# Optimization experiments

Hardware: AMD Instinct MI355X
Metric: run time of the kernel (lower is better)

## Reference

```python
import jax, jax.numpy as jnp
import numpy as np

SEG_LENS = [2048, 8192]
DIL_RATES = [1, 2]


def _dilated_attention(q, k, v, is_causal):
    # q,k,v: [b, n, h, d]
    b, n, h, d = q.shape
    ng = len(SEG_LENS)
    g = h // ng  # heads per group (even split)
    scale = 1.0 / np.sqrt(d).astype(np.float32)
    out = jnp.zeros_like(q)
    for i, (s, r) in enumerate(zip(SEG_LENS, DIL_RATES)):
        hs = i * g
        offset = i % r  # offset_idx % dilation_rate, as in _create_dilation_pattern
        idx = np.arange(offset, s, r)  # dilated positions within a segment, length m
        m = idx.shape[0]
        ns = n // s  # number of segments
        # reshape to segments then gather dilated positions: [b, ns, m, g, d]
        qg = q[:, :, hs:hs + g, :].reshape(b, ns, s, g, d)[:, :, idx]
        kg = k[:, :, hs:hs + g, :].reshape(b, ns, s, g, d)[:, :, idx]
        vg = v[:, :, hs:hs + g, :].reshape(b, ns, s, g, d)[:, :, idx]
        # segment-local attention over dilated tokens only (structured sparsity)
        scores = jnp.einsum('bsqhd,bskhd->bshqk', qg, kg) * scale
        if is_causal:
            cm = np.tril(np.ones((m, m), dtype=bool))  # idx is sorted -> causal in dilated order
            scores = jnp.where(cm, scores, -jnp.inf)
        attn = jax.nn.softmax(scores, axis=-1)
        og = jnp.einsum('bshqk,bskhd->bsqhd', attn, vg)  # [b, ns, m, g, d]
        # scatter back to full segment positions; non-dilated positions stay zero
        full = jnp.zeros((b, ns, s, g, d), q.dtype).at[:, :, idx].set(og)
        out = out.at[:, :, hs:hs + g, :].set(full.reshape(b, n, g, d))
    return out


def setup_inputs() -> dict:
    key = jax.random.key(0)
    k1, k2, k3 = jax.random.split(key, 3)
    shape = (1, 8192, 8, 64)
    q = jax.random.normal(k1, shape, dtype=jnp.float32)
    k = jax.random.normal(k2, shape, dtype=jnp.float32)
    v = jax.random.normal(k3, shape, dtype=jnp.float32)
    return {"q": q, "k": k, "v": v, "is_causal": 1}


def reference(q, k, v, is_causal):
    return _dilated_attention(q, k, v, bool(is_causal))
```

## Files before the change

### kernel.cpp

```cpp
#include <hip/hip_runtime.h>


#define LP 72

typedef __attribute__((ext_vector_type(8))) short bf16x8;
typedef __attribute__((ext_vector_type(4))) float f32x4;
typedef __attribute__((ext_vector_type(4))) unsigned u32x4;
typedef const unsigned int __attribute__((address_space(1)))* gp1;
typedef unsigned int __attribute__((address_space(3)))* lp3;

__device__ __forceinline__ unsigned short f2bf(float f) {
  unsigned u = __builtin_bit_cast(unsigned, f);
  u += 0x7fff + ((u >> 16) & 1);
  return (unsigned short)(u >> 16);
}

__device__ __forceinline__ int region_base(int head) {
  return (head < 4) ? head * 524288 : 2097152 + (head - 4) * 262144;
}

__device__ __forceinline__ void gl_lds16(const unsigned short* g, unsigned short* l) {
  __builtin_amdgcn_global_load_lds((gp1)g, (lp3)l, 16, 0, 0);
}

__global__ __launch_bounds__(256, 4)
void prep_kernel(const float* __restrict__ K, const float* __restrict__ V,
                 unsigned short* __restrict__ Kb, unsigned short* __restrict__ Vt) {
  __shared__ unsigned short sT[64][LP];
  const int bid = blockIdx.x;
  int head, pos0, rate, off;
  if (bid < 512) { head = bid >> 7; pos0 = (bid & 127) * 64; rate = 1; off = 0; }
  else { int b = bid - 512; head = 4 + (b >> 6); pos0 = (b & 63) * 64; rate = 2; off = 1; }
  const int rb = region_base(head);
  const int tid = threadIdx.x;
  const int row = tid >> 2, dg = tid & 3;
  const long tok = (long)(pos0 + row) * rate + off;

  {
    const float* kp = K + tok * 512 + head * 64 + dg * 16;
    unsigned short tmp[16];
    #pragma unroll
    for (int i = 0; i < 4; ++i) {
      float4 f = ((const float4*)kp)[i];
      tmp[i * 4 + 0] = f2bf(f.x); tmp[i * 4 + 1] = f2bf(f.y);
      tmp[i * 4 + 2] = f2bf(f.z); tmp[i * 4 + 3] = f2bf(f.w);
    }
    const int s = row & 7;
    unsigned short* dstrow = Kb + rb + (long)(pos0 + row) * 64;
    *(int4*)(dstrow + (((2 * dg)     ^ s) * 8)) = ((int4*)tmp)[0];
    *(int4*)(dstrow + (((2 * dg + 1) ^ s) * 8)) = ((int4*)tmp)[1];
  }

  {
    const float* vp = V + tok * 512 + head * 64 + dg * 16;
    #pragma unroll
    for (int i = 0; i < 4; ++i) {
      float4 f = ((const float4*)vp)[i];
      unsigned* p = (unsigned*)&sT[row][dg * 16 + i * 4];
      p[0] = (unsigned)f2bf(f.x) | ((unsigned)f2bf(f.y) << 16);
      p[1] = (unsigned)f2bf(f.z) | ((unsigned)f2bf(f.w) << 16);
    }
  }
  __syncthreads();

  {
    const int wv = tid >> 6, lane = tid & 63;
    unsigned pk[8];
    #pragma unroll
    for (int j = 0; j < 8; ++j) {
      unsigned lo = sT[wv * 16 + 2 * j][lane];
      unsigned hi = sT[wv * 16 + 2 * j + 1][lane];
      pk[j] = lo | (hi << 16);
    }
    const int s = lane & 7;
    unsigned short* dstrow = Vt + rb + (long)pos0 * 64 + lane * 64;
    int4 a = {(int)pk[0], (int)pk[1], (int)pk[2], (int)pk[3]};
    int4 b = {(int)pk[4], (int)pk[5], (int)pk[6], (int)pk[7]};
    *(int4*)(dstrow + (((2 * wv)     ^ s) * 8)) = a;
    *(int4*)(dstrow + (((2 * wv + 1) ^ s) * 8)) = b;
  }
}

__global__ __launch_bounds__(256, 2)
void attn_kernel(const float* __restrict__ Q, const unsigned short* __restrict__ Kb,
                 const unsigned short* __restrict__ Vt, const int* __restrict__ IC,
                 float* __restrict__ O, float* __restrict__ Slots) {
  __shared__ __attribute__((aligned(16))) unsigned short sK[2][4096];
  __shared__ __attribute__((aligned(16))) unsigned short sV[2][4096];

  const int bid = blockIdx.x;
  int head, q0, seg0, mseg, rate, off, grp, chunk, slot;
  if (bid < 512) {
    int h4 = bid & 3;
    int u = bid >> 2;
    chunk = u >> 6;
    int t = 63 - (u & 63);
    head = 4 + h4; seg0 = 0; mseg = 4096;
    rate = 2; off = 1; grp = 1;
    q0 = t * 64;
    slot = (h4 * 64 + t) * 2 + chunk;
  } else {
    int cc = bid - 512;
    int job = (cc & 7) | ((cc >> 8) << 3);
    int tloc = (cc & 255) >> 3;
    head = job & 3;
    seg0 = (job >> 2) * 2048;
    q0 = seg0 + tloc * 64; mseg = 2048;
    rate = 1; off = 0; grp = 0; chunk = 0; slot = 0;
  }
  const int rb = region_base(head);
  const bool causal = (*IC) != 0;
  const int tid = threadIdx.x, wave = tid >> 6, lane = tid & 63;
  const int l16 = lane & 15, quad = lane >> 4;
  const int ch0 = ((quad ^ (l16 & 7)) * 8);
  const int ch1 = ch0 ^ 32;

  const int qloc = q0 - seg0;
  const int diagkb = qloc >> 6;
  const int nkb = causal ? diagkb + 1 : (mseg >> 6);
  const int klo = grp ? chunk * 32 : 0;
  const int khi = grp ? min(nkb, klo + 32) : nkb;
  if (klo >= khi) return;

  const float QSCALE = 0.18033688011112042f;
  bf16x8 aQ[2];
  {
    long tok = (long)(q0 + wave * 16 + l16) * rate + off;
    const float* qp = Q + tok * 512 + head * 64 + quad * 8;
    #pragma unroll
    for (int kc = 0; kc < 2; ++kc) {
      float4 f0 = ((const float4*)(qp + kc * 32))[0];
      float4 f1 = ((const float4*)(qp + kc * 32))[1];
      bf16x8 a;
      a[0] = (short)f2bf(f0.x * QSCALE); a[1] = (short)f2bf(f0.y * QSCALE);
      a[2] = (short)f2bf(f0.z * QSCALE); a[3] = (short)f2bf(f0.w * QSCALE);
      a[4] = (short)f2bf(f1.x * QSCALE); a[5] = (short)f2bf(f1.y * QSCALE);
      a[6] = (short)f2bf(f1.z * QSCALE); a[7] = (short)f2bf(f1.w * QSCALE);
      aQ[kc] = a;
    }
  }

  f32x4 oacc[4];
  float lsum = 0.f;
  #pragma unroll
  for (int dt = 0; dt < 4; ++dt) oacc[dt] = (f32x4){0.f, 0.f, 0.f, 0.f};

  const unsigned short* Ksrc = Kb + rb + (long)seg0 * 64;
  const unsigned short* Vsrc = Vt + rb + (long)seg0 * 64;

  const int o0 = wave * 1024;
  const int lo = lane * 8;
  {
    const unsigned short* kt = Ksrc + (long)klo * 4096;
    const unsigned short* vt = Vsrc + (long)klo * 4096;
    gl_lds16(kt + o0 + lo,       &sK[0][o0]);
    gl_lds16(kt + o0 + 512 + lo, &sK[0][o0 + 512]);
    gl_lds16(vt + o0 + lo,       &sV[0][o0]);
    gl_lds16(vt + o0 + 512 + lo, &sV[0][o0 + 512]);
  }

  const int qv = qloc + wave * 16 + l16;

  for (int kb = klo; kb < khi; ++kb) {
    const int cur = (kb - klo) & 1;
    __syncthreads();
    if (kb + 1 < khi) {
      const unsigned short* kt = Ksrc + (long)(kb + 1) * 4096;
      const unsigned short* vt = Vsrc + (long)(kb + 1) * 4096;
      gl_lds16(kt + o0 + lo,       &sK[cur ^ 1][o0]);
      gl_lds16(kt + o0 + 512 + lo, &sK[cur ^ 1][o0 + 512]);
      gl_lds16(vt + o0 + lo,       &sV[cur ^ 1][o0]);
      gl_lds16(vt + o0 + 512 + lo, &sV[cur ^ 1][o0 + 512]);
    }
    const unsigned short* kbuf = &sK[cur][0];
    const unsigned short* vbuf = &sV[cur][0];

    f32x4 sc[4];
    #pragma unroll
    for (int c = 0; c < 4; ++c) {
      const unsigned short* krow = &kbuf[(c * 16 + l16) * 64];
      bf16x8 b0 = *(const bf16x8*)(krow + ch0);
      bf16x8 b1 = *(const bf16x8*)(krow + ch1);
      f32x4 z = (f32x4){0.f, 0.f, 0.f, 0.f};
      z = __builtin_amdgcn_mfma_f32_16x16x32_bf16(b0, aQ[0], z, 0, 0, 0);
      z = __builtin_amdgcn_mfma_f32_16x16x32_bf16(b1, aQ[1], z, 0, 0, 0);
      sc[c] = z;
    }

    float p[4][4];
    if (causal && (kb == diagkb)) {
      #pragma unroll
      for (int c = 0; c < 4; ++c)
        #pragma unroll
        for (int r = 0; r < 4; ++r) {
          float e = __builtin_amdgcn_exp2f(sc[c][r]);
          if (kb * 64 + c * 16 + quad * 4 + r > qv) e = 0.f;
          p[c][r] = e;
        }
    } else {
      #pragma unroll
      for (int c = 0; c < 4; ++c)
        #pragma unroll
        for (int r = 0; r < 4; ++r)
          p[c][r] = __builtin_amdgcn_exp2f(sc[c][r]);
    }

    lsum += (((p[0][0] + p[0][1]) + (p[0][2] + p[0][3])) +
             ((p[1][0] + p[1][1]) + (p[1][2] + p[1][3]))) +
            (((p[2][0] + p[2][1]) + (p[2][2] + p[2][3])) +
             ((p[3][0] + p[3][1]) + (p[3][2] + p[3][3])));

    unsigned W00, W01, W10, W11, W20, W21, W30, W31;
    asm("v_cvt_pk_bf16_f32 %0, %1, %2" : "=v"(W00) : "v"(p[0][0]), "v"(p[0][1]));
    asm("v_cvt_pk_bf16_f32 %0, %1, %2" : "=v"(W01) : "v"(p[0][2]), "v"(p[0][3]));
    asm("v_cvt_pk_bf16_f32 %0, %1, %2" : "=v"(W10) : "v"(p[1][0]), "v"(p[1][1]));
    asm("v_cvt_pk_bf16_f32 %0, %1, %2" : "=v"(W11) : "v"(p[1][2]), "v"(p[1][3]));
    asm("v_cvt_pk_bf16_f32 %0, %1, %2" : "=v"(W20) : "v"(p[2][0]), "v"(p[2][1]));
    asm("v_cvt_pk_bf16_f32 %0, %1, %2" : "=v"(W21) : "v"(p[2][2]), "v"(p[2][3]));
    asm("v_cvt_pk_bf16_f32 %0, %1, %2" : "=v"(W30) : "v"(p[3][0]), "v"(p[3][1]));
    asm("v_cvt_pk_bf16_f32 %0, %1, %2" : "=v"(W31) : "v"(p[3][2]), "v"(p[3][3]));

    unsigned R0 = W00, R2 = W10;
    asm("v_permlane32_swap_b32 %0, %1" : "+v"(R0), "+v"(R2));
    asm("v_permlane16_swap_b32 %0, %1" : "+v"(R0), "+v"(R2));
    unsigned R1 = W01, R3 = W11;
    asm("v_permlane32_swap_b32 %0, %1" : "+v"(R1), "+v"(R3));
    asm("v_permlane16_swap_b32 %0, %1" : "+v"(R1), "+v"(R3));
    unsigned R4 = W20, R6 = W30;
    asm("v_permlane32_swap_b32 %0, %1" : "+v"(R4), "+v"(R6));
    asm("v_permlane16_swap_b32 %0, %1" : "+v"(R4), "+v"(R6));
    unsigned R5 = W21, R7 = W31;
    asm("v_permlane32_swap_b32 %0, %1" : "+v"(R5), "+v"(R7));
    asm("v_permlane16_swap_b32 %0, %1" : "+v"(R5), "+v"(R7));
    u32x4 t0 = {R0, R1, R2, R3};
    u32x4 t1 = {R4, R5, R6, R7};
    bf16x8 pB0 = __builtin_bit_cast(bf16x8, t0);
    bf16x8 pB1 = __builtin_bit_cast(bf16x8, t1);

    #pragma unroll
    for (int dt = 0; dt < 4; ++dt) {
      const unsigned short* vrow = &vbuf[(dt * 16 + l16) * 64];
      bf16x8 v0 = *(const bf16x8*)(vrow + ch0);
      bf16x8 v1 = *(const bf16x8*)(vrow + ch1);
      oacc[dt] = __builtin_amdgcn_mfma_f32_16x16x32_bf16(v0, pB0, oacc[dt], 0, 0, 0);
      oacc[dt] = __builtin_amdgcn_mfma_f32_16x16x32_bf16(v1, pB1, oacc[dt], 0, 0, 0);
    }
  }

  float ltot = lsum;
  ltot += __shfl_xor(ltot, 16);
  ltot += __shfl_xor(ltot, 32);

  if (grp == 1) {
    float* S = Slots + (long)slot * 4160;
    const int qrow = wave * 16 + l16;
    #pragma unroll
    for (int dt = 0; dt < 4; ++dt)
      #pragma unroll
      for (int r = 0; r < 4; ++r)
        S[qrow * 64 + dt * 16 + quad * 4 + r] = oacc[dt][r];
    if (quad == 0) S[4096 + qrow] = ltot;
  } else {
    const int tq = q0 + wave * 16 + l16;
    const float inv = 1.0f / ltot;
    float* dst = O + (long)tq * 512 + head * 64 + quad * 4;
    #pragma unroll
    for (int dt = 0; dt < 4; ++dt)
      #pragma unroll
      for (int r = 0; r < 4; ++r)
        dst[dt * 16 + r] = oacc[dt][r] * inv;
  }
}

__global__ __launch_bounds__(256, 4)
void combine_kernel(const float* __restrict__ Slots, const int* __restrict__ IC,
                    float* __restrict__ O) {
  const int b = blockIdx.x;
  const int h4 = b >> 6, t = b & 63;
  const bool causal = (*IC) != 0;
  const int nkb = causal ? t + 1 : 64;
  const int nc = (nkb > 32) ? 2 : 1;
  const float* s0 = Slots + (long)((h4 * 64 + t) * 2) * 4160;
  const int tid = threadIdx.x;
  const int row = tid >> 2, dq = (tid & 3) * 16;

  float4 acc[4];
  const float4* p0 = (const float4*)(s0 + row * 64 + dq);
  #pragma unroll
  for (int i = 0; i < 4; ++i) acc[i] = p0[i];
  float l = s0[4096 + row];
  if (nc == 2) {
    const float* s1 = s0 + 4160;
    const float4* p1 = (const float4*)(s1 + row * 64 + dq);
    #pragma unroll
    for (int i = 0; i < 4; ++i) {
      float4 v = p1[i];
      acc[i].x += v.x; acc[i].y += v.y; acc[i].z += v.z; acc[i].w += v.w;
    }
    l += s1[4096 + row];
  }
  const float inv = 1.0f / l;
  const long tok = (long)(t * 64 + row) * 2 + 1;
  float* dst = O + tok * 512 + (4 + h4) * 64 + dq;
  #pragma unroll
  for (int i = 0; i < 4; ++i) {
    float4 o = {acc[i].x * inv, acc[i].y * inv, acc[i].z * inv, acc[i].w * inv};
    ((float4*)dst)[i] = o;
  }
  float* dste = O + (tok - 1) * 512 + (4 + h4) * 64 + dq;
  const float4 z = {0.f, 0.f, 0.f, 0.f};
  #pragma unroll
  for (int i = 0; i < 4; ++i) ((float4*)dste)[i] = z;
}

extern "C" void kernel_launch(void* const* d_in, const int* in_sizes, int n_in,
                              void* d_out, int out_size, void* d_ws, size_t ws_size,
                              hipStream_t stream) {
  const float* q = (const float*)d_in[0];
  const float* k = (const float*)d_in[1];
  const float* v = (const float*)d_in[2];
  const int* ic = (const int*)d_in[3];
  unsigned short* Kb = (unsigned short*)d_ws;
  unsigned short* Vt = Kb + 3145728;
  float* Slots = (float*)((char*)d_ws + 12582912);
  prep_kernel<<<dim3(768), dim3(256), 0, stream>>>(k, v, Kb, Vt);
  attn_kernel<<<dim3(1024), dim3(256), 0, stream>>>(q, Kb, Vt, ic, (float*)d_out, Slots);
  combine_kernel<<<dim3(256), dim3(256), 0, stream>>>(Slots, ic, (float*)d_out);
}
```

Measured before the change: 128.9 us.

## Triple-buffer K and split K/V waits to deepen load pipeline

Restructures the attention main loop into a software pipeline where K tiles are triple-buffered and prefetched two blocks ahead, while V is double-buffered and prefetched one ahead. Each iteration now has two barriers with explicit vmcnt waits, one before QK and one before PV, so the V load overlaps the QK/softmax phase instead of both landing before the block starts. This adds LDS usage (an extra 8KB K buffer) and a second barrier per iteration, which could affect occupancy or add sync cost.

```diff
diff --git a/kernel.cpp b/kernel.cpp
--- a/kernel.cpp
+++ b/kernel.cpp
@@ -81,11 +81,15 @@
   }
 }
 
+#define WAITV(n) asm volatile("s_waitcnt vmcnt(" #n ")" ::: "memory")
+#define BARRIER() do { __builtin_amdgcn_s_barrier(); \
+                       __builtin_amdgcn_sched_barrier(0); } while (0)
+
 __global__ __launch_bounds__(256, 2)
 void attn_kernel(const float* __restrict__ Q, const unsigned short* __restrict__ Kb,
                  const unsigned short* __restrict__ Vt, const int* __restrict__ IC,
                  float* __restrict__ O, float* __restrict__ Slots) {
-  __shared__ __attribute__((aligned(16))) unsigned short sK[2][4096];
+  __shared__ __attribute__((aligned(16))) unsigned short sK[3][4096];
   __shared__ __attribute__((aligned(16))) unsigned short sV[2][4096];
 
   const int bid = blockIdx.x;
@@ -150,31 +154,21 @@
 
   const int o0 = wave * 1024;
   const int lo = lane * 8;
-  {
-    const unsigned short* kt = Ksrc + (long)klo * 4096;
-    const unsigned short* vt = Vsrc + (long)klo * 4096;
-    gl_lds16(kt + o0 + lo,       &sK[0][o0]);
-    gl_lds16(kt + o0 + 512 + lo, &sK[0][o0 + 512]);
-    gl_lds16(vt + o0 + lo,       &sV[0][o0]);
-    gl_lds16(vt + o0 + 512 + lo, &sV[0][o0 + 512]);
-  }
-
   const int qv = qloc + wave * 16 + l16;
 
-  for (int kb = klo; kb < khi; ++kb) {
-    const int cur = (kb - klo) & 1;
-    __syncthreads();
-    if (kb + 1 < khi) {
-      const unsigned short* kt = Ksrc + (long)(kb + 1) * 4096;
-      const unsigned short* vt = Vsrc + (long)(kb + 1) * 4096;
-      gl_lds16(kt + o0 + lo,       &sK[cur ^ 1][o0]);
-      gl_lds16(kt + o0 + 512 + lo, &sK[cur ^ 1][o0 + 512]);
-      gl_lds16(vt + o0 + lo,       &sV[cur ^ 1][o0]);
-      gl_lds16(vt + o0 + 512 + lo, &sV[cur ^ 1][o0 + 512]);
-    }
-    const unsigned short* kbuf = &sK[cur][0];
-    const unsigned short* vbuf = &sV[cur][0];
-
+  auto stage_k = [&](int x, int sl) {
+    const unsigned short* kt = Ksrc + (long)x * 4096;
+    gl_lds16(kt + o0 + lo,       &sK[sl][o0]);
+    gl_lds16(kt + o0 + 512 + lo, &sK[sl][o0 + 512]);
+  };
+  auto stage_v = [&](int x) {
+    const unsigned short* vt = Vsrc + (long)x * 4096;
+    gl_lds16(vt + o0 + lo,       &sV[x & 1][o0]);
+    gl_lds16(vt + o0 + 512 + lo, &sV[x & 1][o0 + 512]);
+  };
+
+  struct PB { bf16x8 b0, b1; };
+  auto qk_phase = [&](int kb, const unsigned short* kbuf) -> PB {
     f32x4 sc[4];
     #pragma unroll
     for (int c = 0; c < 4; ++c) {
@@ -234,17 +228,61 @@
     asm("v_permlane16_swap_b32 %0, %1" : "+v"(R5), "+v"(R7));
     u32x4 t0 = {R0, R1, R2, R3};
     u32x4 t1 = {R4, R5, R6, R7};
-    bf16x8 pB0 = __builtin_bit_cast(bf16x8, t0);
-    bf16x8 pB1 = __builtin_bit_cast(bf16x8, t1);
-
+    PB pb;
+    pb.b0 = __builtin_bit_cast(bf16x8, t0);
+    pb.b1 = __builtin_bit_cast(bf16x8, t1);
+    return pb;
+  };
+
+  auto pv_phase = [&](const unsigned short* vbuf, PB pb) {
     #pragma unroll
     for (int dt = 0; dt < 4; ++dt) {
       const unsigned short* vrow = &vbuf[(dt * 16 + l16) * 64];
       bf16x8 v0 = *(const bf16x8*)(vrow + ch0);
       bf16x8 v1 = *(const bf16x8*)(vrow + ch1);
-      oacc[dt] = __builtin_amdgcn_mfma_f32_16x16x32_bf16(v0, pB0, oacc[dt], 0, 0, 0);
-      oacc[dt] = __builtin_amdgcn_mfma_f32_16x16x32_bf16(v1, pB1, oacc[dt], 0, 0, 0);
-    }
+      oacc[dt] = __builtin_amdgcn_mfma_f32_16x16x32_bf16(v0, pb.b0, oacc[dt], 0, 0, 0);
+      oacc[dt] = __builtin_amdgcn_mfma_f32_16x16x32_bf16(v1, pb.b1, oacc[dt], 0, 0, 0);
+    }
+  };
+
+  int kb = klo;
+  int kcur = klo % 3;
+  int ks2 = (klo + 2) % 3;
+  stage_k(klo, kcur);
+  stage_v(klo);
+  if (klo + 1 < khi) stage_k(klo + 1, kcur == 2 ? 0 : kcur + 1);
+
+  while (kb + 2 < khi) {
+    WAITV(4);
+    BARRIER();
+    stage_v(kb + 1);
+    stage_k(kb + 2, ks2);
+    PB pb = qk_phase(kb, &sK[kcur][0]);
+    WAITV(6);
+    BARRIER();
+    pv_phase(&sV[kb & 1][0], pb);
+    ++kb;
+    kcur = kcur == 2 ? 0 : kcur + 1;
+    ks2  = ks2  == 2 ? 0 : ks2  + 1;
+  }
+  if (kb + 1 < khi) {
+    WAITV(4);
+    BARRIER();
+    stage_v(kb + 1);
+    PB pb = qk_phase(kb, &sK[kcur][0]);
+    WAITV(4);
+    BARRIER();
+    pv_phase(&sV[kb & 1][0], pb);
+    ++kb;
+    kcur = kcur == 2 ? 0 : kcur + 1;
+  }
+  {
+    WAITV(2);
+    BARRIER();
+    PB pb = qk_phase(kb, &sK[kcur][0]);
+    WAITV(0);
+    BARRIER();
+    pv_phase(&sV[kb & 1][0], pb);
   }
 
   float ltot = lsum;
```

Result: no change. 130.9 us (+1.5%).

## Load V fragments directly from global into registers, drop V LDS staging

Applied to the files above, without the earlier changes.

The V-transpose kernel now writes V in a fragment-ordered layout that matches the MFMA operand order. The attention loop then reads each lane's eight 16-byte V fragments straight from global memory into registers instead of staging V through double-buffered LDS. This halves LDS use and removes the V LDS reads, which may allow higher occupancy. In exchange, every wave issues redundant global loads of the same V tile each iteration, and those loads sit in the critical path with no prefetch ahead of the QK phase.

```diff
diff --git a/kernel.cpp b/kernel.cpp
--- a/kernel.cpp
+++ b/kernel.cpp
@@ -72,12 +72,13 @@
       unsigned hi = sT[wv * 16 + 2 * j + 1][lane];
       pk[j] = lo | (hi << 16);
     }
-    const int s = lane & 7;
-    unsigned short* dstrow = Vt + rb + (long)pos0 * 64 + lane * 64;
     int4 a = {(int)pk[0], (int)pk[1], (int)pk[2], (int)pk[3]};
     int4 b = {(int)pk[4], (int)pk[5], (int)pk[6], (int)pk[7]};
-    *(int4*)(dstrow + (((2 * wv)     ^ s) * 8)) = a;
-    *(int4*)(dstrow + (((2 * wv + 1) ^ s) * 8)) = b;
+    const int dt = lane >> 4, l16p = lane & 15, h = wv >> 1;
+    const int qa = (wv & 1) * 2, qb = qa + 1;
+    unsigned short* dstc = Vt + rb + (long)pos0 * 64;
+    *(int4*)(dstc + (dt * 2 + h) * 512 + (qa * 16 + l16p) * 8) = a;
+    *(int4*)(dstc + (dt * 2 + h) * 512 + (qb * 16 + l16p) * 8) = b;
   }
 }
 
@@ -86,7 +87,6 @@
                  const unsigned short* __restrict__ Vt, const int* __restrict__ IC,
                  float* __restrict__ O, float* __restrict__ Slots) {
   __shared__ __attribute__((aligned(16))) unsigned short sK[2][4096];
-  __shared__ __attribute__((aligned(16))) unsigned short sV[2][4096];
 
   const int bid = blockIdx.x;
   int head, q0, seg0, mseg, rate, off, grp, chunk, slot;
@@ -150,31 +150,16 @@
 
   const int o0 = wave * 1024;
   const int lo = lane * 8;
-  {
-    const unsigned short* kt = Ksrc + (long)klo * 4096;
-    const unsigned short* vt = Vsrc + (long)klo * 4096;
-    gl_lds16(kt + o0 + lo,       &sK[0][o0]);
-    gl_lds16(kt + o0 + 512 + lo, &sK[0][o0 + 512]);
-    gl_lds16(vt + o0 + lo,       &sV[0][o0]);
-    gl_lds16(vt + o0 + 512 + lo, &sV[0][o0 + 512]);
-  }
-
   const int qv = qloc + wave * 16 + l16;
 
-  for (int kb = klo; kb < khi; ++kb) {
-    const int cur = (kb - klo) & 1;
-    __syncthreads();
-    if (kb + 1 < khi) {
-      const unsigned short* kt = Ksrc + (long)(kb + 1) * 4096;
-      const unsigned short* vt = Vsrc + (long)(kb + 1) * 4096;
-      gl_lds16(kt + o0 + lo,       &sK[cur ^ 1][o0]);
-      gl_lds16(kt + o0 + 512 + lo, &sK[cur ^ 1][o0 + 512]);
-      gl_lds16(vt + o0 + lo,       &sV[cur ^ 1][o0]);
-      gl_lds16(vt + o0 + 512 + lo, &sV[cur ^ 1][o0 + 512]);
-    }
-    const unsigned short* kbuf = &sK[cur][0];
-    const unsigned short* vbuf = &sV[cur][0];
-
+  auto stage_k = [&](int x, int sl) {
+    const unsigned short* kt = Ksrc + (long)x * 4096;
+    gl_lds16(kt + o0 + lo,       &sK[sl][o0]);
+    gl_lds16(kt + o0 + 512 + lo, &sK[sl][o0 + 512]);
+  };
+
+  struct PB { bf16x8 b0, b1; };
+  auto qk_phase = [&](int kb, const unsigned short* kbuf) -> PB {
     f32x4 sc[4];
     #pragma unroll
     for (int c = 0; c < 4; ++c) {
@@ -234,16 +219,34 @@
     asm("v_permlane16_swap_b32 %0, %1" : "+v"(R5), "+v"(R7));
     u32x4 t0 = {R0, R1, R2, R3};
     u32x4 t1 = {R4, R5, R6, R7};
-    bf16x8 pB0 = __builtin_bit_cast(bf16x8, t0);
-    bf16x8 pB1 = __builtin_bit_cast(bf16x8, t1);
+    PB pb;
+    pb.b0 = __builtin_bit_cast(bf16x8, t0);
+    pb.b1 = __builtin_bit_cast(bf16x8, t1);
+    return pb;
+  };
+
+  stage_k(klo, 0);
+
+  for (int kb = klo; kb < khi; ++kb) {
+    const int cur = (kb - klo) & 1;
+    __syncthreads();
+
+    int4 vr[8];
+    {
+      const int4* vt = (const int4*)(Vsrc + (long)kb * 4096);
+      #pragma unroll
+      for (int c = 0; c < 8; ++c) vr[c] = vt[c * 64 + lane];
+    }
+    if (kb + 1 < khi) stage_k(kb + 1, cur ^ 1);
+
+    PB pb = qk_phase(kb, &sK[cur][0]);
 
     #pragma unroll
     for (int dt = 0; dt < 4; ++dt) {
-      const unsigned short* vrow = &vbuf[(dt * 16 + l16) * 64];
-      bf16x8 v0 = *(const bf16x8*)(vrow + ch0);
-      bf16x8 v1 = *(const bf16x8*)(vrow + ch1);
-      oacc[dt] = __builtin_amdgcn_mfma_f32_16x16x32_bf16(v0, pB0, oacc[dt], 0, 0, 0);
-      oacc[dt] = __builtin_amdgcn_mfma_f32_16x16x32_bf16(v1, pB1, oacc[dt], 0, 0, 0);
+      bf16x8 v0 = __builtin_bit_cast(bf16x8, vr[dt * 2]);
+      bf16x8 v1 = __builtin_bit_cast(bf16x8, vr[dt * 2 + 1]);
+      oacc[dt] = __builtin_amdgcn_mfma_f32_16x16x32_bf16(v0, pb.b0, oacc[dt], 0, 0, 0);
+      oacc[dt] = __builtin_amdgcn_mfma_f32_16x16x32_bf16(v1, pb.b1, oacc[dt], 0, 0, 0);
     }
   }
 
```

New measurement: 128.3 us. Within noise of the previous version (-0.5%).
